# Performance work log

Measured on AMD Instinct MI355X. Metric: run time of the kernel, lower is better.

## Reference

```python
import jax, jax.numpy as jnp
import numpy as np

B, N, SEM, STR = 64, 512, 256, 256  # batch, tokens, sem_dim_size, str_dim_size (hidden=512)


def setup_inputs() -> dict:
    key = jax.random.key(0)
    ks = jax.random.split(key, 8)
    s = 0.02  # small init so exp(f_ij)/exp(f_i) stay well-conditioned
    return {
        "input": jax.random.normal(ks[0], (B, N, SEM + STR), jnp.float32),
        "Wp": (jax.random.normal(ks[1], (STR, STR), jnp.float32) * s),
        "bp": jnp.zeros((STR,), jnp.float32),
        "Wbil": (jax.random.normal(ks[2], (STR, STR), jnp.float32) * s),
        "bbil": jnp.zeros((), jnp.float32),
        "Wfi": (jax.random.normal(ks[3], (1, STR), jnp.float32) * s),
        "bfi": jnp.zeros((1,), jnp.float32),
        "exparam": jax.random.normal(ks[4], (1, 1, SEM), jnp.float32),
        "Wfz": (jax.random.normal(ks[5], (SEM, 2 * SEM), jnp.float32) * s),
        "bfz": jnp.zeros((SEM,), jnp.float32),
    }


def reference(input, Wp, bp, Wbil, bbil, Wfi, bfi, exparam, Wfz, bfz):
    b, n, _ = input.shape
    sem_v = input[:, :, :SEM]          # [B,N,SEM]
    str_v = input[:, :, SEM:]          # [B,N,STR]

    # NOTE: source uses tp_linear for BOTH tp and tc, and expands both with
    # unsqueeze(2), so f_ij[b,i,j] = bilinear(tp[b,i], tp[b,i]) is constant in j.
    tp = str_v @ Wp.T + bp             # [B,N,STR]
    s = jnp.einsum('bid,de,bie->bi', tp, Wbil, tp) + bbil   # [B,N]
    f_ij = jnp.broadcast_to(s[:, :, None], (b, n, n))        # [B,N,N]

    f_i = jnp.exp(str_v @ Wfi.T + bfi)[..., 0]               # [B,N]

    off = 1.0 - jnp.eye(n, dtype=input.dtype)
    A = jnp.exp(f_ij) * off                                  # zero diagonal
    deg = jnp.sum(A, axis=2)                                 # [B,N]
    L = -A + deg[:, :, None] * jnp.eye(n, dtype=input.dtype) # Laplacian
    L = L.at[:, 0, :].set(f_i)                               # root-augmented L_bar

    LLinv = jnp.linalg.inv(L)                                # [B,N,N]
    d0 = f_i * LLinv[:, :, 0]                                # root marginals [B,N]
    dg = jnp.diagonal(LLinv, axis1=-2, axis2=-1)             # [B,N]

    # tmp1 and tmp2 in the source both reduce to A[b,i,j] * diag[b,j]
    tmp = A * dg[:, None, :]
    mask1 = jnp.concatenate([jnp.zeros((n, 1)), jnp.ones((n, n - 1))], 1).astype(input.dtype)
    mask2 = jnp.concatenate([jnp.zeros((1, n)), jnp.ones((n - 1, n))], 0).astype(input.dtype)
    dx = (mask1 - mask2) * tmp                               # [B,N,N]

    d = jnp.concatenate([d0[:, None, :], dx], axis=1)        # [B,N+1,N]
    df = jnp.swapaxes(d, 1, 2)                               # [B,N,N+1]
    ssr = jnp.concatenate([jnp.broadcast_to(exparam, (b, 1, SEM)), sem_v], 1)  # [B,N+1,SEM]
    pinp = jnp.einsum('bnm,bmd->bnd', df, ssr)               # [B,N,SEM]
    # cinp = dx @ sem_v is computed in the source but never used -> omitted

    finp = jnp.concatenate([sem_v, pinp], axis=-1)           # [B,N,2*SEM]
    return jax.nn.relu(finp @ Wfz.T + bfz)                   # [B,N,SEM]
```

## Files before the change

### kernel.cpp

```cpp
#include <hip/hip_runtime.h>
#include <math.h>

#define B_    64
#define N_    512
#define SEM_  256
#define STR_  256
#define DIM_  512
#define ROWS_ (B_*N_)

#define OFF_T      0
#define OFF_QT16   65536
#define OFF_W116   98304
#define OFF_W2T    131072
#define OFF_V1     196608
#define OFF_C1     196864
#define OFF_H      197120
#define OFF_C0     197376
#define OFF_EV     197440
#define OFF_FV     230208
#define OFF_SUMP   262976
#define OFF_V2B    394048
#define OFF_ROW0   410432

typedef __bf16 bf16x8 __attribute__((ext_vector_type(8)));
typedef float  f32x4  __attribute__((ext_vector_type(4)));

__device__ __forceinline__ ushort f2b(float x) {
    return __builtin_bit_cast(ushort, (__bf16)x);
}
__device__ __forceinline__ float b2f(ushort h) {
    unsigned u = ((unsigned)h) << 16;
    return __builtin_bit_cast(float, u);
}

__global__ __launch_bounds__(256) void k0a(
    const float* __restrict__ Wp, const float* __restrict__ bp,
    const float* __restrict__ Wbil, const float* __restrict__ Wfz,
    const float* __restrict__ exparam,
    float* __restrict__ T, ushort* __restrict__ W116, float* __restrict__ W2t,
    float* __restrict__ v1, float* __restrict__ h, float* __restrict__ c0)
{
    int t = threadIdx.x, a = blockIdx.x;
    float acc = 0.f;
    const float* wb = Wbil + a*256;
    for (int c = 0; c < 256; ++c) acc += wb[c] * Wp[c*256 + t];
    T[a*256 + t] = acc;
    W116[a*256 + t] = f2b(Wfz[a*512 + t]);
    W2t[t*256 + a] = Wfz[a*512 + 256 + t];
    if (a == 0) {
        float s = 0.f;
        const float* w2 = Wfz + t*512 + 256;
        for (int dd = 0; dd < 256; ++dd) s += w2[dd] * exparam[dd];
        v1[t] = s;
    }
    if (a == 1) {
        float g = 0.f, g2 = 0.f;
        for (int c = 0; c < 256; ++c) {
            g  += Wbil[t*256 + c] * bp[c];
            g2 += Wbil[c*256 + t] * bp[c];
        }
        h[t] = g + g2;
        __shared__ float red[256];
        red[t] = bp[t] * g;
        __syncthreads();
        for (int s2 = 128; s2 > 0; s2 >>= 1) {
            if (t < s2) red[t] += red[t + s2];
            __syncthreads();
        }
        if (t == 0) c0[0] = red[0];
    }
}

__global__ __launch_bounds__(256) void k0b(
    const float* __restrict__ Wp, const float* __restrict__ T,
    const float* __restrict__ h,
    ushort* __restrict__ Qt16, float* __restrict__ c1)
{
    int t = threadIdx.x, d = blockIdx.x;
    float acc = 0.f;
    for (int a2 = 0; a2 < 256; ++a2) acc += Wp[a2*256 + d] * T[a2*256 + t];
    Qt16[t*256 + d] = f2b(acc);
    __shared__ float red[256];
    red[t] = Wp[t*256 + d] * h[t];
    __syncthreads();
    for (int s2 = 128; s2 > 0; s2 >>= 1) {
        if (t < s2) red[t] += red[t + s2];
        __syncthreads();
    }
    if (t == 0) c1[d] = red[0];
}

__global__ __launch_bounds__(256) void k_rowstats(
    const float* __restrict__ input, const ushort* __restrict__ Qt16,
    const float* __restrict__ c1, const float* __restrict__ c0,
    const float* __restrict__ Wfi, const float* __restrict__ bbil,
    const float* __restrict__ bfi, const float* __restrict__ W2t,
    float* __restrict__ Ev, float* __restrict__ fv, float* __restrict__ v2b)
{
    __shared__ __align__(16) ushort Ash[64][264];
    __shared__ __align__(16) ushort Bs[256][40];
    __shared__ float sred[64][4];
    __shared__ float fred[64][4];
    __shared__ float s0sh[256];
    __shared__ float shE0;
    int t = threadIdx.x;
    int lane = t & 63, w = t >> 6;
    int g = lane >> 4, li = lane & 15;
    long rowbase = (long)blockIdx.x * 64;
    int b = (int)(rowbase >> 9);
    int i0 = (int)(rowbase & 511);
    const float* Ab = input + rowbase*DIM_ + SEM_;

#pragma unroll
    for (int q = 0; q < 16; ++q) {
        int v = t + 256*q;
        int r = v >> 6, c4 = v & 63;
        float4 a4 = *(const float4*)(Ab + (long)r*DIM_ + c4*4);
        ushort4 b4 = make_ushort4(f2b(a4.x), f2b(a4.y), f2b(a4.z), f2b(a4.w));
        *(ushort4*)&Ash[r][c4*4] = b4;
    }

    f32x4 acc[4][4];
#pragma unroll
    for (int m = 0; m < 4; ++m)
#pragma unroll
        for (int n = 0; n < 4; ++n) acc[m][n] = (f32x4){0.f, 0.f, 0.f, 0.f};

    for (int k0 = 0; k0 < 256; k0 += 32) {
#pragma unroll
        for (int q = 0; q < 4; ++q) {
            int v = t + 256*q;
            int n = v >> 2, c = v & 3;
            *(uint4*)&Bs[n][c*8] = *(const uint4*)&Qt16[n*256 + k0 + c*8];
        }
        __syncthreads();
        bf16x8 af[4], bfr[4];
#pragma unroll
        for (int m = 0; m < 4; ++m)
            af[m] = *(const bf16x8*)&Ash[m*16 + li][k0 + g*8];
#pragma unroll
        for (int n = 0; n < 4; ++n)
            bfr[n] = *(const bf16x8*)&Bs[w*64 + n*16 + li][g*8];
#pragma unroll
        for (int m = 0; m < 4; ++m)
#pragma unroll
            for (int n = 0; n < 4; ++n)
                acc[m][n] = __builtin_amdgcn_mfma_f32_16x16x32_bf16(af[m], bfr[n], acc[m][n], 0, 0, 0);
        __syncthreads();
    }

    float c1v[4], wfv[4];
#pragma unroll
    for (int n = 0; n < 4; ++n) {
        int col = w*64 + n*16 + li;
        c1v[n] = c1[col];
        wfv[n] = Wfi[col];
    }
#pragma unroll
    for (int m = 0; m < 4; ++m) {
#pragma unroll
        for (int reg = 0; reg < 4; ++reg) {
            int row = m*16 + g*4 + reg;
            float sp = 0.f, fp = 0.f;
#pragma unroll
            for (int n = 0; n < 4; ++n) {
                int col = w*64 + n*16 + li;
                float sv = b2f(Ash[row][col]);
                sp += (acc[m][n][reg] + c1v[n]) * sv;
                fp += wfv[n] * sv;
            }
#pragma unroll
            for (int off = 1; off < 16; off <<= 1) {
                sp += __shfl_xor(sp, off);
                fp += __shfl_xor(fp, off);
            }
            if (li == 0) { sred[row][w] = sp; fred[row][w] = fp; }
        }
    }
    __syncthreads();
    if (t < 64) {
        float ss = sred[t][0] + sred[t][1] + sred[t][2] + sred[t][3];
        float ff = fred[t][0] + fred[t][1] + fred[t][2] + fred[t][3];
        float ev = expf(ss + c0[0] + bbil[0]);
        Ev[rowbase + t] = ev;
        fv[rowbase + t] = expf(ff + bfi[0]);
        if (t == 0) shE0 = ev;
    }

    if (i0 == 0) {
        if (t < 64)
            *(float4*)&s0sh[t*4] = *(const float4*)(input + (long)b*512*DIM_ + t*4);
        __syncthreads();
        float a2 = 0.f;
        for (int d = 0; d < 256; ++d) a2 += W2t[d*256 + t] * s0sh[d];
        v2b[b*256 + t] = shE0 * a2;
    }
}

__global__ __launch_bounds__(256) void k_final(
    const float* __restrict__ input, const ushort* __restrict__ W116,
    const float* __restrict__ v1, const float* __restrict__ v2b,
    const float* __restrict__ Ev, const float* __restrict__ fv,
    const float* __restrict__ bfz,
    float* __restrict__ sump, float* __restrict__ row0pre,
    float* __restrict__ out)
{
    __shared__ __align__(16) ushort Ash[64][264];
    __shared__ __align__(16) ushort Bs[256][40];
    __shared__ float cAs[64], cBs[64];
    __shared__ float EvL[64];
    __shared__ float redF[256];
    int t = threadIdx.x;
    int lane = t & 63, w = t >> 6;
    int g = lane >> 4, li = lane & 15;
    long rowbase = (long)blockIdx.x * 64;
    int b = (int)(rowbase >> 9);
    int i0 = (int)(rowbase & 511);
    const float* Ab = input + rowbase*DIM_;

    redF[t] = fv[b*512 + t] + fv[b*512 + 256 + t];
    __syncthreads();
    for (int s2 = 128; s2 > 0; s2 >>= 1) {
        if (t < s2) redF[t] += redF[t + s2];
        __syncthreads();
    }
    float invF = 1.0f / redF[0];
    __syncthreads();

    if (t < 64) {
        int row = (int)rowbase + t;
        float fr = fv[row];
        float ev = Ev[row];
        EvL[t] = ev;
        cAs[t] = fr * invF;
        cBs[t] = ((i0 + t) == 0) ? -invF
               : (1.0f + (fv[b*512] - fr)*invF) / (512.0f * ev);
    }

#pragma unroll
    for (int q = 0; q < 16; ++q) {
        int v = t + 256*q;
        int r = v >> 6, c4 = v & 63;
        float4 a4 = *(const float4*)(Ab + (long)r*DIM_ + c4*4);
        ushort4 b4 = make_ushort4(f2b(a4.x), f2b(a4.y), f2b(a4.z), f2b(a4.w));
        *(ushort4*)&Ash[r][c4*4] = b4;
    }

    f32x4 acc[4][4];
#pragma unroll
    for (int m = 0; m < 4; ++m)
#pragma unroll
        for (int n = 0; n < 4; ++n) acc[m][n] = (f32x4){0.f, 0.f, 0.f, 0.f};

    for (int k0 = 0; k0 < 256; k0 += 32) {
#pragma unroll
        for (int q = 0; q < 4; ++q) {
            int v = t + 256*q;
            int n = v >> 2, c = v & 3;
            *(uint4*)&Bs[n][c*8] = *(const uint4*)&W116[n*256 + k0 + c*8];
        }
        __syncthreads();
        bf16x8 af[4], bfr[4];
#pragma unroll
        for (int m = 0; m < 4; ++m)
            af[m] = *(const bf16x8*)&Ash[m*16 + li][k0 + g*8];
#pragma unroll
        for (int n = 0; n < 4; ++n)
            bfr[n] = *(const bf16x8*)&Bs[w*64 + n*16 + li][g*8];
#pragma unroll
        for (int m = 0; m < 4; ++m)
#pragma unroll
            for (int n = 0; n < 4; ++n)
                acc[m][n] = __builtin_amdgcn_mfma_f32_16x16x32_bf16(af[m], bfr[n], acc[m][n], 0, 0, 0);
        __syncthreads();
    }

    {
        float sp = 0.f;
        int rstart = (i0 == 0) ? 1 : 0;
        for (int r = rstart; r < 64; ++r) sp += EvL[r] * b2f(Ash[r][t]);
        sump[(long)blockIdx.x*256 + t] = sp;
    }

    float v1v[4], v2v[4], bzv[4];
#pragma unroll
    for (int n = 0; n < 4; ++n) {
        int col = w*64 + n*16 + li;
        v1v[n] = v1[col];
        v2v[n] = v2b[b*256 + col];
        bzv[n] = bfz[col];
    }

    __syncthreads();
    float* Csh = (float*)&Ash[0][0];
#pragma unroll
    for (int hh = 0; hh < 2; ++hh) {
#pragma unroll
        for (int mm = 0; mm < 2; ++mm) {
            int m = hh*2 + mm;
#pragma unroll
            for (int reg = 0; reg < 4; ++reg) {
                int row = m*16 + g*4 + reg;
                float ca = cAs[row], cb = cBs[row];
                int irow = i0 + row;
#pragma unroll
                for (int n = 0; n < 4; ++n) {
                    int col = w*64 + n*16 + li;
                    float sel = (irow == 0) ? 0.f : v2v[n];
                    float val = acc[m][n][reg] + ca*v1v[n] + cb*sel + bzv[n];
                    if (irow == 0) row0pre[b*256 + col] = val;
                    Csh[(row - hh*32)*264 + col] = fmaxf(val, 0.f);
                }
            }
        }
        __syncthreads();
#pragma unroll
        for (int q = 0; q < 8; ++q) {
            int v = t + 256*q;
            int r = v >> 6, c4 = v & 63;
            *(float4*)(out + (rowbase + hh*32 + r)*256 + c4*4) = *(const float4*)&Csh[r*264 + c4*4];
        }
        __syncthreads();
    }
}

__global__ __launch_bounds__(256) void k_fix(
    const float* __restrict__ sump, const float* __restrict__ fv,
    const float* __restrict__ W2t, const float* __restrict__ row0pre,
    float* __restrict__ out)
{
    int b = blockIdx.x, t = threadIdx.x;
    __shared__ float svsh[256];
    __shared__ float redF[256];
    float a = 0.f;
#pragma unroll
    for (int p = 0; p < 8; ++p) a += sump[(long)(b*8 + p)*256 + t];
    svsh[t] = a;
    redF[t] = fv[b*512 + t] + fv[b*512 + 256 + t];
    __syncthreads();
    for (int s2 = 128; s2 > 0; s2 >>= 1) {
        if (t < s2) redF[t] += redF[t + s2];
        __syncthreads();
    }
    float invF = 1.0f / redF[0];
    float a0 = 0.f;
    for (int d = 0; d < 256; ++d) a0 += W2t[d*256 + t] * svsh[d];
    out[((long)b*512)*256 + t] = fmaxf(row0pre[b*256 + t] - invF*a0, 0.f);
}

extern "C" void kernel_launch(void* const* d_in, const int* in_sizes, int n_in,
                              void* d_out, int out_size, void* d_ws, size_t ws_size,
                              hipStream_t stream) {
    const float* input   = (const float*)d_in[0];
    const float* Wp      = (const float*)d_in[1];
    const float* bp      = (const float*)d_in[2];
    const float* Wbil    = (const float*)d_in[3];
    const float* bbil    = (const float*)d_in[4];
    const float* Wfi     = (const float*)d_in[5];
    const float* bfi     = (const float*)d_in[6];
    const float* exparam = (const float*)d_in[7];
    const float* Wfz     = (const float*)d_in[8];
    const float* bfz     = (const float*)d_in[9];
    float* ws  = (float*)d_ws;
    float* out = (float*)d_out;

    float*  T     = ws + OFF_T;
    ushort* Qt16  = (ushort*)(ws + OFF_QT16);
    ushort* W116  = (ushort*)(ws + OFF_W116);
    float*  W2t   = ws + OFF_W2T;
    float*  v1    = ws + OFF_V1;
    float*  c1    = ws + OFF_C1;
    float*  h     = ws + OFF_H;
    float*  c0    = ws + OFF_C0;
    float*  Ev    = ws + OFF_EV;
    float*  fv    = ws + OFF_FV;
    float*  sump  = ws + OFF_SUMP;
    float*  v2b   = ws + OFF_V2B;
    float*  row0p = ws + OFF_ROW0;

    k0a<<<256, 256, 0, stream>>>(Wp, bp, Wbil, Wfz, exparam, T, W116, W2t, v1, h, c0);
    k0b<<<256, 256, 0, stream>>>(Wp, T, h, Qt16, c1);
    k_rowstats<<<ROWS_/64, 256, 0, stream>>>(input, Qt16, c1, c0, Wfi, bbil, bfi, W2t, Ev, fv, v2b);
    k_final<<<ROWS_/64, 256, 0, stream>>>(input, W116, v1, v2b, Ev, fv, bfz, sump, row0p, out);
    k_fix<<<B_, 256, 0, stream>>>(sump, fv, W2t, row0p, out);
}
```

Measured before the change: 93.80 us.

## Swizzle shared tiles and compute row dot products with MFMA

Replaces the padded row-major shared A tile with an XOR-swizzled unpadded layout in both GEMM kernels, to cut LDS bank conflicts on the fragment loads. In k_rowstats, the per-row bilinear and Wfi dot products are no longer done with scalar loops and shuffles. The GEMM result is written back to LDS as bf16 and the dot products are taken from the diagonal of extra MFMA products. In k_final, the weighted column sum becomes a vectorized two-stage reduction, a wave-shuffle replaces the tree reduction, and one barrier is moved. Storing the intermediate as bf16 adds rounding error to the bilinear score.

```diff
diff --git a/kernel.cpp b/kernel.cpp
--- a/kernel.cpp
+++ b/kernel.cpp
@@ -31,6 +31,12 @@
 __device__ __forceinline__ float b2f(ushort h) {
     unsigned u = ((unsigned)h) << 16;
     return __builtin_bit_cast(float, u);
+}
+__device__ __forceinline__ float bflo(unsigned u) {
+    return __builtin_bit_cast(float, u << 16);
+}
+__device__ __forceinline__ float bfhi(unsigned u) {
+    return __builtin_bit_cast(float, u & 0xffff0000u);
 }
 
 __global__ __launch_bounds__(256) void k0a(
@@ -97,12 +103,15 @@
     const float* __restrict__ bfi, const float* __restrict__ W2t,
     float* __restrict__ Ev, float* __restrict__ fv, float* __restrict__ v2b)
 {
-    __shared__ __align__(16) ushort Ash[64][264];
-    __shared__ __align__(16) ushort Bs[256][40];
-    __shared__ float sred[64][4];
-    __shared__ float fred[64][4];
-    __shared__ float s0sh[256];
-    __shared__ float shE0;
+    __shared__ __align__(16) char smem[69632];
+    ushort* Ash   = (ushort*)smem;
+    ushort* Bsm   = (ushort*)(smem + 32768);
+    ushort* Ush   = (ushort*)(smem + 32768);
+    float*  sdiag = (float*)(smem + 65536);
+    float*  fdiag = (float*)(smem + 66560);
+    float*  s0sh  = (float*)(smem + 67584);
+    float*  shE0  = (float*)(smem + 68608);
+
     int t = threadIdx.x;
     int lane = t & 63, w = t >> 6;
     int g = lane >> 4, li = lane & 15;
@@ -117,7 +126,7 @@
         int r = v >> 6, c4 = v & 63;
         float4 a4 = *(const float4*)(Ab + (long)r*DIM_ + c4*4);
         ushort4 b4 = make_ushort4(f2b(a4.x), f2b(a4.y), f2b(a4.z), f2b(a4.w));
-        *(ushort4*)&Ash[r][c4*4] = b4;
+        *(ushort4*)&Ash[r*256 + ((c4*4) ^ ((r & 7) << 3))] = b4;
     }
 
     f32x4 acc[4][4];
@@ -131,16 +140,17 @@
         for (int q = 0; q < 4; ++q) {
             int v = t + 256*q;
             int n = v >> 2, c = v & 3;
-            *(uint4*)&Bs[n][c*8] = *(const uint4*)&Qt16[n*256 + k0 + c*8];
+            *(uint4*)&Bsm[n*40 + c*8] = *(const uint4*)&Qt16[n*256 + k0 + c*8];
         }
         __syncthreads();
         bf16x8 af[4], bfr[4];
+        int xs = (li & 7) << 3;
 #pragma unroll
         for (int m = 0; m < 4; ++m)
-            af[m] = *(const bf16x8*)&Ash[m*16 + li][k0 + g*8];
+            af[m] = *(const bf16x8*)&Ash[(m*16 + li)*256 + ((k0 + g*8) ^ xs)];
 #pragma unroll
         for (int n = 0; n < 4; ++n)
-            bfr[n] = *(const bf16x8*)&Bs[w*64 + n*16 + li][g*8];
+            bfr[n] = *(const bf16x8*)&Bsm[(w*64 + n*16 + li)*40 + g*8];
 #pragma unroll
         for (int m = 0; m < 4; ++m)
 #pragma unroll
@@ -149,42 +159,61 @@
         __syncthreads();
     }
 
-    float c1v[4], wfv[4];
-#pragma unroll
-    for (int n = 0; n < 4; ++n) {
-        int col = w*64 + n*16 + li;
-        c1v[n] = c1[col];
-        wfv[n] = Wfi[col];
-    }
-#pragma unroll
-    for (int m = 0; m < 4; ++m) {
-#pragma unroll
-        for (int reg = 0; reg < 4; ++reg) {
-            int row = m*16 + g*4 + reg;
-            float sp = 0.f, fp = 0.f;
-#pragma unroll
-            for (int n = 0; n < 4; ++n) {
+    float c1v[4];
+#pragma unroll
+    for (int n = 0; n < 4; ++n) c1v[n] = c1[w*64 + n*16 + li];
+#pragma unroll
+    for (int m = 0; m < 4; ++m)
+#pragma unroll
+        for (int n = 0; n < 4; ++n)
+#pragma unroll
+            for (int reg = 0; reg < 4; ++reg) {
+                int row = m*16 + g*4 + reg;
                 int col = w*64 + n*16 + li;
-                float sv = b2f(Ash[row][col]);
-                sp += (acc[m][n][reg] + c1v[n]) * sv;
-                fp += wfv[n] * sv;
+                Ush[row*256 + (col ^ ((row & 7) << 3))] = f2b(acc[m][n][reg] + c1v[n]);
             }
-#pragma unroll
-            for (int off = 1; off < 16; off <<= 1) {
-                sp += __shfl_xor(sp, off);
-                fp += __shfl_xor(fp, off);
-            }
-            if (li == 0) { sred[row][w] = sp; fred[row][w] = fp; }
-        }
+    __syncthreads();
+
+    f32x4 dacc[4], facc[4];
+#pragma unroll
+    for (int m = 0; m < 4; ++m) { dacc[m] = (f32x4){0.f,0.f,0.f,0.f}; facc[m] = (f32x4){0.f,0.f,0.f,0.f}; }
+#pragma unroll
+    for (int kk = 0; kk < 2; ++kk) {
+        int kb = (w*2 + kk)*32 + g*8;
+        float4 wf0 = *(const float4*)(Wfi + kb);
+        float4 wf1 = *(const float4*)(Wfi + kb + 4);
+        bf16x8 afw = (bf16x8){(__bf16)wf0.x, (__bf16)wf0.y, (__bf16)wf0.z, (__bf16)wf0.w,
+                              (__bf16)wf1.x, (__bf16)wf1.y, (__bf16)wf1.z, (__bf16)wf1.w};
+        int xs = (li & 7) << 3;
+#pragma unroll
+        for (int m = 0; m < 4; ++m) {
+            int ridx = (m*16 + li)*256 + (kb ^ xs);
+            bf16x8 afu = *(const bf16x8*)&Ush[ridx];
+            bf16x8 bfs = *(const bf16x8*)&Ash[ridx];
+            dacc[m] = __builtin_amdgcn_mfma_f32_16x16x32_bf16(afu, bfs, dacc[m], 0, 0, 0);
+            facc[m] = __builtin_amdgcn_mfma_f32_16x16x32_bf16(afw, bfs, facc[m], 0, 0, 0);
+        }
+    }
+    if (g == (li >> 2)) {
+        int dr = li & 3;
+#pragma unroll
+        for (int m = 0; m < 4; ++m) {
+            float dv = dr == 0 ? dacc[m][0] : dr == 1 ? dacc[m][1] : dr == 2 ? dacc[m][2] : dacc[m][3];
+            sdiag[(m*16 + li)*4 + w] = dv;
+        }
+    }
+    if (g == 0) {
+#pragma unroll
+        for (int m = 0; m < 4; ++m) fdiag[(m*16 + li)*4 + w] = facc[m][0];
     }
     __syncthreads();
     if (t < 64) {
-        float ss = sred[t][0] + sred[t][1] + sred[t][2] + sred[t][3];
-        float ff = fred[t][0] + fred[t][1] + fred[t][2] + fred[t][3];
+        float ss = sdiag[t*4] + sdiag[t*4+1] + sdiag[t*4+2] + sdiag[t*4+3];
+        float ff = fdiag[t*4] + fdiag[t*4+1] + fdiag[t*4+2] + fdiag[t*4+3];
         float ev = expf(ss + c0[0] + bbil[0]);
         Ev[rowbase + t] = ev;
         fv[rowbase + t] = expf(ff + bfi[0]);
-        if (t == 0) shE0 = ev;
+        if (t == 0) shE0[0] = ev;
     }
 
     if (i0 == 0) {
@@ -193,7 +222,7 @@
         __syncthreads();
         float a2 = 0.f;
         for (int d = 0; d < 256; ++d) a2 += W2t[d*256 + t] * s0sh[d];
-        v2b[b*256 + t] = shE0 * a2;
+        v2b[b*256 + t] = shE0[0] * a2;
     }
 }
 
@@ -205,11 +234,16 @@
     float* __restrict__ sump, float* __restrict__ row0pre,
     float* __restrict__ out)
 {
-    __shared__ __align__(16) ushort Ash[64][264];
-    __shared__ __align__(16) ushort Bs[256][40];
-    __shared__ float cAs[64], cBs[64];
-    __shared__ float EvL[64];
-    __shared__ float redF[256];
+    __shared__ __align__(16) char smem[62976];
+    ushort* Ash    = (ushort*)smem;
+    ushort* Bsm    = (ushort*)(smem + 32768);
+    float*  Csh    = (float*)smem;
+    float*  sumred = (float*)(smem + 53248);
+    float*  cAs    = (float*)(smem + 61440);
+    float*  cBs    = (float*)(smem + 61696);
+    float*  EvL    = (float*)(smem + 61952);
+    float*  wred   = (float*)(smem + 62208);
+
     int t = threadIdx.x;
     int lane = t & 63, w = t >> 6;
     int g = lane >> 4, li = lane & 15;
@@ -218,20 +252,18 @@
     int i0 = (int)(rowbase & 511);
     const float* Ab = input + rowbase*DIM_;
 
-    redF[t] = fv[b*512 + t] + fv[b*512 + 256 + t];
-    __syncthreads();
-    for (int s2 = 128; s2 > 0; s2 >>= 1) {
-        if (t < s2) redF[t] += redF[t + s2];
-        __syncthreads();
-    }
-    float invF = 1.0f / redF[0];
-    __syncthreads();
+    float fsum = fv[b*512 + t] + fv[b*512 + 256 + t];
+#pragma unroll
+    for (int off = 32; off >= 1; off >>= 1) fsum += __shfl_down(fsum, off);
+    if (lane == 0) wred[w] = fsum;
+    __syncthreads();
+    float invF = 1.0f / (wred[0] + wred[1] + wred[2] + wred[3]);
 
     if (t < 64) {
         int row = (int)rowbase + t;
         float fr = fv[row];
         float ev = Ev[row];
-        EvL[t] = ev;
+        EvL[t] = (i0 == 0 && t == 0) ? 0.f : ev;
         cAs[t] = fr * invF;
         cBs[t] = ((i0 + t) == 0) ? -invF
                : (1.0f + (fv[b*512] - fr)*invF) / (512.0f * ev);
@@ -243,7 +275,7 @@
         int r = v >> 6, c4 = v & 63;
         float4 a4 = *(const float4*)(Ab + (long)r*DIM_ + c4*4);
         ushort4 b4 = make_ushort4(f2b(a4.x), f2b(a4.y), f2b(a4.z), f2b(a4.w));
-        *(ushort4*)&Ash[r][c4*4] = b4;
+        *(ushort4*)&Ash[r*256 + ((c4*4) ^ ((r & 7) << 3))] = b4;
     }
 
     f32x4 acc[4][4];
@@ -257,16 +289,17 @@
         for (int q = 0; q < 4; ++q) {
             int v = t + 256*q;
             int n = v >> 2, c = v & 3;
-            *(uint4*)&Bs[n][c*8] = *(const uint4*)&W116[n*256 + k0 + c*8];
+            *(uint4*)&Bsm[n*40 + c*8] = *(const uint4*)&W116[n*256 + k0 + c*8];
         }
         __syncthreads();
         bf16x8 af[4], bfr[4];
+        int xs = (li & 7) << 3;
 #pragma unroll
         for (int m = 0; m < 4; ++m)
-            af[m] = *(const bf16x8*)&Ash[m*16 + li][k0 + g*8];
+            af[m] = *(const bf16x8*)&Ash[(m*16 + li)*256 + ((k0 + g*8) ^ xs)];
 #pragma unroll
         for (int n = 0; n < 4; ++n)
-            bfr[n] = *(const bf16x8*)&Bs[w*64 + n*16 + li][g*8];
+            bfr[n] = *(const bf16x8*)&Bsm[(w*64 + n*16 + li)*40 + g*8];
 #pragma unroll
         for (int m = 0; m < 4; ++m)
 #pragma unroll
@@ -276,9 +309,28 @@
     }
 
     {
+        int qq = t >> 5, c8 = t & 31;
+        float p[8];
+#pragma unroll
+        for (int i = 0; i < 8; ++i) p[i] = 0.f;
+#pragma unroll
+        for (int rr = 0; rr < 8; ++rr) {
+            int r = qq*8 + rr;
+            float ev = EvL[r];
+            uint4 uv = *(const uint4*)&Ash[r*256 + ((c8*8) ^ (rr << 3))];
+            p[0] += ev * bflo(uv.x); p[1] += ev * bfhi(uv.x);
+            p[2] += ev * bflo(uv.y); p[3] += ev * bfhi(uv.y);
+            p[4] += ev * bflo(uv.z); p[5] += ev * bfhi(uv.z);
+            p[6] += ev * bflo(uv.w); p[7] += ev * bfhi(uv.w);
+        }
+        *(float4*)&sumred[qq*256 + c8*8]     = (float4){p[0], p[1], p[2], p[3]};
+        *(float4*)&sumred[qq*256 + c8*8 + 4] = (float4){p[4], p[5], p[6], p[7]};
+    }
+    __syncthreads();
+    {
         float sp = 0.f;
-        int rstart = (i0 == 0) ? 1 : 0;
-        for (int r = rstart; r < 64; ++r) sp += EvL[r] * b2f(Ash[r][t]);
+#pragma unroll
+        for (int qq = 0; qq < 8; ++qq) sp += sumred[qq*256 + t];
         sump[(long)blockIdx.x*256 + t] = sp;
     }
 
@@ -291,10 +343,9 @@
         bzv[n] = bfz[col];
     }
 
-    __syncthreads();
-    float* Csh = (float*)&Ash[0][0];
 #pragma unroll
     for (int hh = 0; hh < 2; ++hh) {
+        __syncthreads();
 #pragma unroll
         for (int mm = 0; mm < 2; ++mm) {
             int m = hh*2 + mm;
@@ -320,7 +371,6 @@
             int r = v >> 6, c4 = v & 63;
             *(float4*)(out + (rowbase + hh*32 + r)*256 + c4*4) = *(const float4*)&Csh[r*264 + c4*4];
         }
-        __syncthreads();
     }
 }
 
```

Measured after the change: 88.98 us. 5.1% less time.
